# Kernel tuning notes

Measured on AMD Instinct MI355X. Metric: run time of the kernel, lower is better.

## Reference

```python
import jax, jax.numpy as jnp
import numpy as np

MAX_INT = 1e4  # sentinel used by the original (transitions into START / out of STOP forbidden)
VOCAB, E, H, T, B, S = 50257, 512, 1024, 50, 8, 512  # T = tagset_size + 2


def _lstm_scan(x, h0, c0, Wih, Whh, b):
    # x: [time, batch, E] (time axis is the ORIGINAL batch dim, faithful to the
    # torch code which feeds [B,S,E] into a batch_first=False LSTM)
    def step(carry, xt):
        h, c = carry
        g = xt @ Wih.T + h @ Whh.T + b
        i, f, gg, o = jnp.split(g, 4, axis=-1)  # torch gate order i,f,g,o
        c = jax.nn.sigmoid(f) * c + jax.nn.sigmoid(i) * jnp.tanh(gg)
        h = jax.nn.sigmoid(o) * jnp.tanh(c)
        return (h, c), h
    _, hs = jax.lax.scan(step, (h0, c0), x)
    return hs


def setup_inputs() -> dict:
    key = jax.random.key(0)
    k = jax.random.split(key, 14)
    Hd = H // 2
    X = jax.random.randint(k[0], (B, S), 0, VOCAB)
    Y = jax.random.randint(k[1], (B, S), 0, T - 2)  # real tags only (no start/stop)
    h0 = jax.random.normal(k[2], (2, S, Hd), jnp.float32)
    c0 = jax.random.normal(k[3], (2, S, Hd), jnp.float32)
    emb_table = jax.random.normal(k[4], (VOCAB, E), jnp.float32) * 0.02
    Wih_f = jax.random.normal(k[5], (4 * Hd, E), jnp.float32) * 0.05
    Whh_f = jax.random.normal(k[6], (4 * Hd, Hd), jnp.float32) * 0.05
    b_f = jnp.zeros((4 * Hd,), jnp.float32)
    Wih_b = jax.random.normal(k[7], (4 * Hd, E), jnp.float32) * 0.05
    Whh_b = jax.random.normal(k[8], (4 * Hd, Hd), jnp.float32) * 0.05
    b_b = jnp.zeros((4 * Hd,), jnp.float32)
    fc_W = jax.random.normal(k[9], (T, H), jnp.float32) * 0.05
    fc_b = jnp.zeros((T,), jnp.float32)
    tr = jax.random.normal(k[10], (T, T), jnp.float32)
    transitions = tr.at[-2, :].set(-MAX_INT).at[:, -1].set(-MAX_INT)
    return {"X": X, "Y": Y, "h0": h0, "c0": c0, "emb_table": emb_table,
            "Wih_f": Wih_f, "Whh_f": Whh_f, "b_f": b_f,
            "Wih_b": Wih_b, "Whh_b": Whh_b, "b_b": b_b,
            "fc_W": fc_W, "fc_b": fc_b, "transitions": transitions}


def reference(X, Y, h0, c0, emb_table, Wih_f, Whh_f, b_f, Wih_b, Whh_b, b_b, fc_W, fc_b, transitions):
    emb = emb_table[X]                                   # [B,S,E]
    # BiLSTM: torch sees axis0 as time (faithful quirk), hidden batch == S
    hf = _lstm_scan(emb, h0[0], c0[0], Wih_f, Whh_f, b_f)
    hb = _lstm_scan(emb[::-1], h0[1], c0[1], Wih_b, Whh_b, b_b)[::-1]
    lstm_out = jnp.concatenate([hf, hb], axis=-1)        # [B,S,H]
    feats = lstm_out @ fc_W.T + fc_b                     # [B,S,T]
    nB, Tt = X.shape[0], transitions.shape[0]
    # CRF forward algorithm (log partition), vectorized over tags
    init = jnp.full((nB, Tt), -MAX_INT, feats.dtype).at[:, -2].set(0.0)
    def crf_step(fv, feat):                              # fv [B,T], feat [B,T]
        nv = fv[:, None, :] + transitions[None, :, :] + feat[:, :, None]  # [B,next,prev]
        return jax.nn.logsumexp(nv, axis=2), None
    fv, _ = jax.lax.scan(crf_step, init, jnp.swapaxes(feats, 0, 1))
    forward_score = jax.nn.logsumexp(fv + transitions[-1][None, :], axis=1).sum()
    # gold path score
    start = jnp.full((nB, 1), Tt - 2, dtype=Y.dtype)
    tags = jnp.concatenate([start, Y], axis=1)           # [B,S+1]
    trans_sc = transitions[tags[:, 1:], tags[:, :-1]].sum()
    emit_sc = jnp.take_along_axis(feats, tags[:, 1:, None], axis=2)[..., 0].sum()
    gold_score = trans_sc + emit_sc + transitions[-1, tags[:, -1]].sum()
    score = forward_score - gold_score
    return score, Y
```

## Files before the change

### kernel.cpp

```cpp
#include <hip/hip_runtime.h>
#include <hip/hip_bf16.h>

typedef __attribute__((ext_vector_type(4))) float f32x4;
typedef __attribute__((ext_vector_type(8))) short short8;

#define LN2F 0.69314718055994531f

__device__ __forceinline__ unsigned short f2b(float x){
  union{float f;unsigned u;}v; v.f=x;
  unsigned r = v.u + 0x7fffu + ((v.u>>16)&1u);
  return (unsigned short)(r>>16);
}
__device__ __forceinline__ float b2f(unsigned short h){
  union{unsigned u;float f;}v; v.u = ((unsigned)h)<<16; return v.f;
}
__device__ __forceinline__ float sigm(float x){ return 1.f/(1.f+__expf(-x)); }
__device__ __forceinline__ float tanh_(float x){ float t=__expf(2.f*x); return 1.f - 2.f/(t+1.f); }

__device__ __forceinline__ void gll16(const void* g, void* l){
  __builtin_amdgcn_global_load_lds((const __attribute__((address_space(1))) void*)g,
                                   (__attribute__((address_space(3))) void*)l, 16, 0, 0);
}

__global__ __launch_bounds__(256) void prep_kernel(
  const int* __restrict__ X, const int* __restrict__ Y,
  const float* __restrict__ h0, const float* __restrict__ c0,
  const float* __restrict__ emb,
  const float* __restrict__ WihF, const float* __restrict__ WihB,
  const float* __restrict__ WhhFf, const float* __restrict__ WhhBf,
  const float* __restrict__ fcWf, const float* __restrict__ trans,
  unsigned short* __restrict__ Abf, unsigned short* __restrict__ Wcat,
  unsigned short* __restrict__ WhhF, unsigned short* __restrict__ WhhB,
  unsigned short* __restrict__ hbufs, float* __restrict__ cbuf,
  unsigned short* __restrict__ fcW, unsigned short* __restrict__ Ebf,
  float* __restrict__ out)
{
  const int tid = blockIdx.x*256 + threadIdx.x;
  const int nth = gridDim.x*256;
  if(tid==0) out[0] = 0.f;
  for(int i=tid;i<524288;i+=nth){
    int r = i>>7, q = i&127;
    float4 v = ((const float4*)(emb + (size_t)X[r]*512))[q];
    ushort4 o; o.x=f2b(v.x); o.y=f2b(v.y); o.z=f2b(v.z); o.w=f2b(v.w);
    ((ushort4*)Abf)[i] = o;
  }
  for(int i=tid;i<524288;i+=nth){
    int r = i>>7, q = i&127;
    const float* src = (r<2048) ? (WihF + (size_t)r*512) : (WihB + (size_t)(r-2048)*512);
    float4 v = ((const float4*)src)[q];
    ushort4 o; o.x=f2b(v.x); o.y=f2b(v.y); o.z=f2b(v.z); o.w=f2b(v.w);
    ((ushort4*)Wcat)[i] = o;
  }
  for(int i=tid;i<262144;i+=nth){
    float4 v = ((const float4*)WhhFf)[i];
    ushort4 o; o.x=f2b(v.x); o.y=f2b(v.y); o.z=f2b(v.z); o.w=f2b(v.w);
    ((ushort4*)WhhF)[i] = o;
  }
  for(int i=tid;i<262144;i+=nth){
    float4 v = ((const float4*)WhhBf)[i];
    ushort4 o; o.x=f2b(v.x); o.y=f2b(v.y); o.z=f2b(v.z); o.w=f2b(v.w);
    ((ushort4*)WhhB)[i] = o;
  }
  for(int i=tid;i<131072;i+=nth){
    int d = i>>16, rest = i&65535;
    float4 v = ((const float4*)h0)[i];
    ushort4 o; o.x=f2b(v.x); o.y=f2b(v.y); o.z=f2b(v.z); o.w=f2b(v.w);
    ((ushort4*)hbufs)[(size_t)(d*2)*65536 + rest] = o;
  }
  for(int i=tid;i<131072;i+=nth) ((float4*)cbuf)[i] = ((const float4*)c0)[i];
  for(int i=tid;i<16384;i+=nth){
    int n = i>>8, q = i&255;
    float4 v;
    if (n<50) v = ((const float4*)(fcWf + (size_t)n*1024))[q];
    else { v.x=0.f; v.y=0.f; v.z=0.f; v.w=0.f; }
    ushort4 o; o.x=f2b(v.x); o.y=f2b(v.y); o.z=f2b(v.z); o.w=f2b(v.w);
    ((ushort4*)fcW)[i] = o;
  }
  for(int i=tid;i<4096;i+=nth){
    int n = i>>6, p = i&63;
    float v = (n<50 && p<50) ? __expf(trans[n*50+p]) : 0.f;
    Ebf[i] = f2b(v);
  }
  for(int i=tid;i<4096;i+=nth) out[1+i] = (float)Y[i];
}

__global__ __launch_bounds__(256) void gemm1_kernel(const unsigned short* __restrict__ A,
                                                    const unsigned short* __restrict__ B,
                                                    unsigned short* __restrict__ C){
  __shared__ __align__(16) unsigned short SS[4][4][2][2048];
  const int t = threadIdx.x, w = t>>6, l = t&63;
  const int m0 = blockIdx.x<<7, n0 = blockIdx.y<<7;
  const int wr = (w>>1)<<6, wc = (w&1)<<6;
  const int fr = l&15, fk = (l>>4)<<3;
  const int sr = l>>2, c0 = (l&3)<<3;
  f32x4 acc[4][4];
  #pragma unroll
  for(int i=0;i<4;i++)
    #pragma unroll
    for(int j=0;j<4;j++) acc[i][j]=(f32x4)0.f;
  const unsigned short* Aw = A + (size_t)(m0+wr)*512;
  const unsigned short* Bw = B + (size_t)(n0+wc)*512;
#define G1STAGE(KT) { \
    unsigned short* pa_ = &SS[w][(KT)&3][0][0]; \
    unsigned short* pb_ = &SS[w][(KT)&3][1][0]; \
    const int kc_ = ((KT)<<5) + c0; \
    gll16(Aw + (size_t)(    sr)*512 + kc_, pa_); \
    gll16(Aw + (size_t)(16+sr)*512 + kc_, pa_+512); \
    gll16(Aw + (size_t)(32+sr)*512 + kc_, pa_+1024); \
    gll16(Aw + (size_t)(48+sr)*512 + kc_, pa_+1536); \
    gll16(Bw + (size_t)(    sr)*512 + kc_, pb_); \
    gll16(Bw + (size_t)(16+sr)*512 + kc_, pb_+512); \
    gll16(Bw + (size_t)(32+sr)*512 + kc_, pb_+1024); \
    gll16(Bw + (size_t)(48+sr)*512 + kc_, pb_+1536); \
  }
  G1STAGE(0) G1STAGE(1) G1STAGE(2)
#define G1STEP(KT, VM) { \
    if((KT)+3 < 16) G1STAGE((KT)+3) \
    asm volatile("s_waitcnt vmcnt(" VM ")" ::: "memory"); \
    const unsigned short* pa_ = &SS[w][(KT)&3][0][0]; \
    const unsigned short* pb_ = &SS[w][(KT)&3][1][0]; \
    short8 af_[4], bf_[4]; \
    _Pragma("unroll") \
    for(int mi=0;mi<4;mi++) af_[mi] = *(const short8*)(pa_ + mi*512 + fr*32 + fk); \
    _Pragma("unroll") \
    for(int ni=0;ni<4;ni++) bf_[ni] = *(const short8*)(pb_ + ni*512 + fr*32 + fk); \
    _Pragma("unroll") \
    for(int mi=0;mi<4;mi++) \
      _Pragma("unroll") \
      for(int ni=0;ni<4;ni++) \
        acc[mi][ni] = __builtin_amdgcn_mfma_f32_16x16x32_bf16(af_[mi], bf_[ni], acc[mi][ni], 0,0,0); \
  }
  G1STEP(0,"24")  G1STEP(1,"24")  G1STEP(2,"24")  G1STEP(3,"24")
  G1STEP(4,"24")  G1STEP(5,"24")  G1STEP(6,"24")  G1STEP(7,"24")
  G1STEP(8,"24")  G1STEP(9,"24")  G1STEP(10,"24") G1STEP(11,"24")
  G1STEP(12,"24") G1STEP(13,"16") G1STEP(14,"8")  G1STEP(15,"0")
#undef G1STEP
#undef G1STAGE
  #pragma unroll
  for(int mi=0;mi<4;mi++)
    #pragma unroll
    for(int ni=0;ni<4;ni++)
      #pragma unroll
      for(int j=0;j<4;j++){
        int row = m0 + wr + mi*16 + ((l>>4)<<2) + j;
        int col = n0 + wc + ni*16 + fr;
        C[(size_t)row*4096 + col] = f2b(acc[mi][ni][j]);
      }
}

__global__ __launch_bounds__(256) void lstm_step_kernel(
  unsigned short* __restrict__ hbufs, float* __restrict__ cbuf,
  unsigned short* __restrict__ hall, const unsigned short* __restrict__ Gin,
  const unsigned short* __restrict__ WhhF_, const unsigned short* __restrict__ WhhB_,
  const float* __restrict__ bF, const float* __restrict__ bB, int t)
{
  __shared__ __align__(16) unsigned short WL[16*4*64*8];
  __shared__ __align__(16) unsigned short Ab4[4][128*32];
  const int d = blockIdx.z;
  const int m0 = blockIdx.x<<7;
  const int u0 = blockIdx.y<<4;
  const int tin = d ? (7-t) : t;
  const int par = t&1;
  const unsigned short* hprev = hbufs + (size_t)(d*2+par)*262144;
  unsigned short* hnext = hbufs + (size_t)(d*2+(par^1))*262144;
  const unsigned short* W = d ? WhhB_ : WhhF_;
  const float* bias = d ? bB : bF;
  const int tx = threadIdx.x, w = tx>>6, l = tx&63;
  const int fr = l&15, q = l>>4, fk = q<<3;
  {
    const int row = tx >> 2, qq = tx & 3;
    const int g = row >> 4, ul = row & 15;
    const int grow = (g<<9) + u0 + ul;
    #pragma unroll
    for(int kt=0;kt<16;kt++){
      uint4 v = *(const uint4*)(W + (size_t)grow*512 + kt*32 + qq*8);
      *(uint4*)(WL + ((kt*4+g)*64 + (qq*16+ul))*8) = v;
    }
  }
  __syncthreads();
  f32x4 acc[2][4];
  #pragma unroll
  for(int i=0;i<2;i++)
    #pragma unroll
    for(int j=0;j<4;j++) acc[i][j]=(f32x4)0.f;
  const int r0 = (w<<5) + (l>>2), c0 = (l&3)<<3;
  const unsigned short* hA0 = hprev + (size_t)(m0+r0)*512;
  const unsigned short* hA1 = hprev + (size_t)(m0+r0+16)*512;
#define ABUF(i) (Ab4[(i)] + ((w<<5)*32))
  gll16(hA0 + 0*32 + c0, ABUF(0)); gll16(hA1 + 0*32 + c0, ABUF(0)+16*32);
  gll16(hA0 + 1*32 + c0, ABUF(1)); gll16(hA1 + 1*32 + c0, ABUF(1)+16*32);
  gll16(hA0 + 2*32 + c0, ABUF(2)); gll16(hA1 + 2*32 + c0, ABUF(2)+16*32);
#define LSTEP(KT, VM) {                                                       \
    if((KT)+3 < 16){                                                          \
      const int kc_ = ((KT)+3)*32 + c0;                                       \
      gll16(hA0 + kc_, ABUF(((KT)+3)&3));                                     \
      gll16(hA1 + kc_, ABUF(((KT)+3)&3)+16*32);                               \
    }                                                                         \
    asm volatile("s_waitcnt vmcnt(" VM ")" ::: "memory");                     \
    const unsigned short* cur_ = ABUF((KT)&3);                                \
    short8 a0_ = *(const short8*)(cur_ + fr*32 + fk);                         \
    short8 a1_ = *(const short8*)(cur_ + (16+fr)*32 + fk);                    \
    short8 bv_[4];                                                            \
    _Pragma("unroll")                                                         \
    for(int g=0;g<4;g++) bv_[g] = *(const short8*)(WL + (((KT)*4+g)*64 + l)*8);\
    _Pragma("unroll")                                                         \
    for(int g=0;g<4;g++){                                                     \
      acc[0][g] = __builtin_amdgcn_mfma_f32_16x16x32_bf16(a0_, bv_[g], acc[0][g], 0,0,0); \
      acc[1][g] = __builtin_amdgcn_mfma_f32_16x16x32_bf16(a1_, bv_[g], acc[1][g], 0,0,0); \
    }                                                                         \
  }
  LSTEP(0,"6")  LSTEP(1,"6")  LSTEP(2,"6")  LSTEP(3,"6")
  LSTEP(4,"6")  LSTEP(5,"6")  LSTEP(6,"6")  LSTEP(7,"6")
  LSTEP(8,"6")  LSTEP(9,"6")  LSTEP(10,"6") LSTEP(11,"6")
  LSTEP(12,"6") LSTEP(13,"4") LSTEP(14,"2") LSTEP(15,"0")
#undef LSTEP
#undef ABUF
  #pragma unroll
  for(int mi=0;mi<2;mi++)
    #pragma unroll
    for(int j=0;j<4;j++){
      int rs = m0 + w*32 + mi*16 + (q<<2) + j;
      int u  = u0 + fr;
      size_t grow = (size_t)(tin*512 + rs)*4096 + (size_t)d*2048;
      float p0 = acc[mi][0][j] + b2f(Gin[grow +    0 + u]) + bias[   0+u];
      float p1 = acc[mi][1][j] + b2f(Gin[grow +  512 + u]) + bias[ 512+u];
      float p2 = acc[mi][2][j] + b2f(Gin[grow + 1024 + u]) + bias[1024+u];
      float p3 = acc[mi][3][j] + b2f(Gin[grow + 1536 + u]) + bias[1536+u];
      size_t ci = (size_t)d*262144 + (size_t)rs*512 + u;
      float c = sigm(p1)*cbuf[ci] + sigm(p0)*tanh_(p2);
      cbuf[ci] = c;
      float h = sigm(p3)*tanh_(c);
      hnext[(size_t)rs*512+u] = f2b(h);
      hall[(size_t)(tin*512+rs)*1024 + (size_t)d*512 + u] = f2b(h);
    }
}

__global__ __launch_bounds__(256) void fc_kernel(const unsigned short* __restrict__ hA,
    const unsigned short* __restrict__ Wf, const float* __restrict__ fcb,
    float* __restrict__ feats){
  __shared__ __align__(16) unsigned short As[128*40];
  __shared__ __align__(16) unsigned short Bs[64*40];
  const int tx = threadIdx.x, w = tx>>6, l = tx&63;
  const int m0 = blockIdx.x<<7;
  const int srow = tx>>2, scol = (tx&3)<<3;
  const int fr=l&15, fk=(l>>4)<<3;
  f32x4 acc[2][4];
  #pragma unroll
  for(int i=0;i<2;i++)
    #pragma unroll
    for(int j=0;j<4;j++) acc[i][j]=(f32x4)0.f;
  uint4 pa0 = *(const uint4*)(hA + (size_t)(m0+srow)*1024 + scol);
  uint4 pa1 = *(const uint4*)(hA + (size_t)(m0+64+srow)*1024 + scol);
  uint4 pb0 = *(const uint4*)(Wf + (size_t)srow*1024 + scol);
  for(int kt=0; kt<32; ++kt){
    __syncthreads();
    *(uint4*)&As[srow*40+scol] = pa0;
    *(uint4*)&As[(64+srow)*40+scol] = pa1;
    *(uint4*)&Bs[srow*40+scol] = pb0;
    __syncthreads();
    if(kt<31){
      int kc = (kt+1)*32 + scol;
      pa0 = *(const uint4*)(hA + (size_t)(m0+srow)*1024 + kc);
      pa1 = *(const uint4*)(hA + (size_t)(m0+64+srow)*1024 + kc);
      pb0 = *(const uint4*)(Wf + (size_t)srow*1024 + kc);
    }
    short8 af[2], bf[4];
    #pragma unroll
    for(int mi=0;mi<2;mi++) af[mi] = *(const short8*)&As[(w*32+mi*16+fr)*40 + fk];
    #pragma unroll
    for(int ni=0;ni<4;ni++) bf[ni] = *(const short8*)&Bs[(ni*16+fr)*40 + fk];
    #pragma unroll
    for(int mi=0;mi<2;mi++)
      #pragma unroll
      for(int ni=0;ni<4;ni++)
        acc[mi][ni] = __builtin_amdgcn_mfma_f32_16x16x32_bf16(af[mi], bf[ni], acc[mi][ni], 0,0,0);
  }
  #pragma unroll
  for(int mi=0;mi<2;mi++)
    #pragma unroll
    for(int ni=0;ni<4;ni++)
      #pragma unroll
      for(int j=0;j<4;j++){
        int rs = m0 + w*32 + mi*16 + ((l>>4)<<2) + j;
        int n  = ni*16 + fr;
        feats[(size_t)rs*64+n] = acc[mi][ni][j] + (n<50 ? fcb[n] : 0.f);
      }
}

__global__ __launch_bounds__(64) void crf_group_kernel(
    const float* __restrict__ feats, const unsigned short* __restrict__ Ebf,
    float* __restrict__ Wout, int* __restrict__ kexp)
{
  __shared__ __align__(16) unsigned short PT[64*72];
  __shared__ float fe[32*64];
  const int g = blockIdx.x, b = blockIdx.y;
  const int l = threadIdx.x;
  const int lj = l & 15, q = l >> 4;
  const float* fb = feats + (size_t)(b*512 + g*32)*64;
  #pragma unroll
  for(int j=0;j<32;j++) fe[j*64 + l] = fb[j*64 + l];
  short8 afE[4][2];
  #pragma unroll
  for(int i=0;i<4;i++)
    #pragma unroll
    for(int h=0;h<2;h++)
      afE[i][h] = *(const short8*)(Ebf + (i*16+lj)*64 + h*32 + q*8);
  {
    uint4 erow[8];
    #pragma unroll
    for(int i=0;i<8;i++) erow[i] = *(const uint4*)(Ebf + l*64 + i*8);
    float ef0 = __expf(fe[l]);
    const unsigned* e32 = (const unsigned*)erow;
    #pragma unroll
    for(int m=0;m<64;m++){
      unsigned short eb = (unsigned short)(e32[m>>1] >> ((m&1)*16));
      PT[m*72 + l] = f2b(b2f(eb) * ef0);
    }
  }
  float sc_lag = 1.f;
  int exprev = 0, kblk = 0;
  for(int k=1;k<32;k++){
    kblk += exprev;
    float ev[4][4];
    #pragma unroll
    for(int i=0;i<4;i++)
      #pragma unroll
      for(int r=0;r<4;r++)
        ev[i][r] = __expf(fe[k*64 + i*16 + q*4 + r]) * sc_lag;
    short8 bfP[4][2];
    #pragma unroll
    for(int j=0;j<4;j++)
      #pragma unroll
      for(int h=0;h<2;h++)
        bfP[j][h] = *(const short8*)&PT[(j*16+lj)*72 + h*32 + q*8];
    f32x4 acc[4][4];
    #pragma unroll
    for(int i=0;i<4;i++)
      #pragma unroll
      for(int j=0;j<4;j++) acc[i][j] = (f32x4)0.f;
    #pragma unroll
    for(int h=0;h<2;h++)
      #pragma unroll
      for(int i=0;i<4;i++)
        #pragma unroll
        for(int j=0;j<4;j++)
          acc[i][j] = __builtin_amdgcn_mfma_f32_16x16x32_bf16(afE[i][h], bfP[j][h], acc[i][j], 0,0,0);
    float mx = 1e-30f;
    float* Wo = Wout + (size_t)(b*16 + g)*4096;
    #pragma unroll
    for(int i=0;i<4;i++)
      #pragma unroll
      for(int j=0;j<4;j++){
        float v0 = acc[i][j][0]*ev[i][0];
        float v1 = acc[i][j][1]*ev[i][1];
        float v2 = acc[i][j][2]*ev[i][2];
        float v3 = acc[i][j][3]*ev[i][3];
        mx = fmaxf(fmaxf(mx, fmaxf(v0,v1)), fmaxf(v2,v3));
        int base = (j*16+lj)*72 + i*16 + q*4;
        *(unsigned*)&PT[base]   = (unsigned)f2b(v0) | ((unsigned)f2b(v1)<<16);
        *(unsigned*)&PT[base+2] = (unsigned)f2b(v2) | ((unsigned)f2b(v3)<<16);
        if(k==31){
          int n = i*16 + q*4, m = j*16 + lj;
          Wo[(size_t)(n+0)*64 + m] = v0;
          Wo[(size_t)(n+1)*64 + m] = v1;
          Wo[(size_t)(n+2)*64 + m] = v2;
          Wo[(size_t)(n+3)*64 + m] = v3;
        }
      }
    #pragma unroll
    for(int off=1; off<64; off<<=1) mx = fmaxf(mx, __shfl_xor(mx, off));
    int ex = ((__builtin_bit_cast(int, mx) >> 23) & 0xff) - 127;
    ex = ex < -120 ? -120 : (ex > 120 ? 120 : ex);
    sc_lag = __builtin_bit_cast(float, (unsigned)((127-ex)<<23));
    exprev = ex;
  }
  if(l==0) kexp[b*16 + g] = kblk;
}

__global__ __launch_bounds__(256) void crf_seq_kernel(const float* __restrict__ W,
    const int* __restrict__ kexp, const float* __restrict__ trans,
    const float* __restrict__ feats, const int* __restrict__ Y,
    float* __restrict__ out){
  const int b = blockIdx.x;
  if(b < 8){
    if(threadIdx.x >= 64) return;
    __shared__ __align__(16) float sh[64];
    const int l = threadIdx.x;
    const float* Wb = W + (size_t)b*65536;
    float kl = (l<16) ? (float)kexp[b*16 + l] : 0.f;
    #pragma unroll
    for(int off=32;off;off>>=1) kl += __shfl_down(kl, off);
    float G = (l==48) ? 1.f : 0.f;
    float sc = 1.f, Mrun = 0.f;
    int exprev = 0;
    float4 curA[16], curB[16];
    #pragma unroll
    for(int i=0;i<16;i++) curA[i] = ((const float4*)(Wb + (size_t)l*64))[i];

#define SEQ_STEP(CUR, NXT, GI) {                                            \
    sh[l] = G;                                                              \
    const float* wn = Wb + (size_t)(((GI)+1)&15)*4096 + (size_t)l*64;       \
    _Pragma("unroll")                                                       \
    for(int i=0;i<16;i++) NXT[i] = ((const float4*)wn)[i];                  \
    float4 gq[16];                                                          \
    _Pragma("unroll")                                                       \
    for(int i=0;i<16;i++) gq[i] = ((const float4*)sh)[i];                   \
    float a0=0.f,a1=0.f,a2=0.f,a3=0.f;                                      \
    _Pragma("unroll")                                                       \
    for(int i=0;i<16;i++){                                                  \
      a0 = fmaf(CUR[i].x, gq[i].x, a0);                                     \
      a1 = fmaf(CUR[i].y, gq[i].y, a1);                                     \
      a2 = fmaf(CUR[i].z, gq[i].z, a2);                                     \
      a3 = fmaf(CUR[i].w, gq[i].w, a3);                                     \
    }                                                                       \
    float S = (a0+a1)+(a2+a3);                                              \
    Mrun += (float)exprev;                                                  \
    G = S * sc;                                                             \
    float Sp = __builtin_bit_cast(float, __builtin_amdgcn_readfirstlane(    \
                 __builtin_bit_cast(int, fmaxf(S, 1e-35f))));               \
    int ex = ((__builtin_bit_cast(int, Sp) >> 23) & 0xff) - 127;            \
    ex = ex < -120 ? -120 : (ex > 120 ? 120 : ex);                          \
    sc = __builtin_bit_cast(float, (unsigned)((127-ex)<<23));               \
    exprev = ex;                                                            \
  }

    for(int g=0; g<16; g+=2){
      SEQ_STEP(curA, curB, g)
      SEQ_STEP(curB, curA, g+1)
    }
#undef SEQ_STEP
    float u = (l<50) ? __expf(trans[49*50+l]) : 0.f;
    float val = G * u;
    #pragma unroll
    for(int off=32;off;off>>=1) val += __shfl_down(val, off);
    if(l==0) atomicAdd(out, logf(fmaxf(val,1e-35f)) + (Mrun + kl)*LN2F);
  } else {
    const int tx = threadIdx.x;
    float acc = 0.f;
    for(int i=tx; i<4096; i+=256){
      int s = i & 511;
      int y = Y[i];
      int prev = s ? Y[i-1] : 48;
      acc += trans[y*50+prev] + feats[(size_t)i*64+y];
      if (s==511) acc += trans[49*50+y];
    }
    #pragma unroll
    for(int off=32; off; off>>=1) acc += __shfl_down(acc, off);
    __shared__ float red[4];
    if((tx&63)==0) red[tx>>6] = acc;
    __syncthreads();
    if(tx==0) atomicAdd(out, -(red[0]+red[1]+red[2]+red[3]));
  }
}

extern "C" void kernel_launch(void* const* d_in, const int* in_sizes, int n_in,
                              void* d_out, int out_size, void* d_ws, size_t ws_size,
                              hipStream_t stream) {
  (void)in_sizes; (void)n_in; (void)out_size; (void)ws_size;
  const int*   X     = (const int*)d_in[0];
  const int*   Y     = (const int*)d_in[1];
  const float* h0    = (const float*)d_in[2];
  const float* c0    = (const float*)d_in[3];
  const float* emb   = (const float*)d_in[4];
  const float* WihF  = (const float*)d_in[5];
  const float* WhhFf = (const float*)d_in[6];
  const float* bF    = (const float*)d_in[7];
  const float* WihB  = (const float*)d_in[8];
  const float* WhhBf = (const float*)d_in[9];
  const float* bB    = (const float*)d_in[10];
  const float* fcWf  = (const float*)d_in[11];
  const float* fcb   = (const float*)d_in[12];
  const float* trans = (const float*)d_in[13];
  float* out = (float*)d_out;
  char* ws = (char*)d_ws;

  unsigned short* Abf   = (unsigned short*)(ws + 0);
  unsigned short* Wcat  = (unsigned short*)(ws + 4194304);
  unsigned short* WhhF  = (unsigned short*)(ws + 8388608);
  unsigned short* WhhB  = (unsigned short*)(ws + 10485760);
  unsigned short* Gin   = (unsigned short*)(ws + 12582912);
  float*          Wgrp  = (float*)(ws + 12582912);
  int*            kexp  = (int*)(ws + 20971520);
  unsigned short* hbufs = (unsigned short*)(ws + 46137344);
  float*          cbuf  = (float*)(ws + 48234496);
  unsigned short* hall  = (unsigned short*)(ws + 50331648);
  unsigned short* fcW   = (unsigned short*)(ws + 58720256);
  float*          feats = (float*)(ws + 58851328);
  unsigned short* Ebf   = (unsigned short*)(ws + 59900160);

  hipLaunchKernelGGL(prep_kernel, dim3(1024), dim3(256), 0, stream,
      X, Y, h0, c0, emb, WihF, WihB, WhhFf, WhhBf, fcWf, trans,
      Abf, Wcat, WhhF, WhhB, hbufs, cbuf, fcW, Ebf, out);
  hipLaunchKernelGGL(gemm1_kernel, dim3(32,32), dim3(256), 0, stream, Abf, Wcat, Gin);
  for(int t=0;t<8;t++)
    hipLaunchKernelGGL(lstm_step_kernel, dim3(4,32,2), dim3(256), 0, stream,
        hbufs, cbuf, hall, Gin, WhhF, WhhB, bF, bB, t);
  hipLaunchKernelGGL(fc_kernel, dim3(32), dim3(256), 0, stream, hall, fcW, fcb, feats);
  hipLaunchKernelGGL(crf_group_kernel, dim3(16,8), dim3(64), 0, stream, feats, Ebf, Wgrp, kexp);
  hipLaunchKernelGGL(crf_seq_kernel, dim3(9), dim3(256), 0, stream, Wgrp, kexp, trans, feats, Y, out);
}
```

Measured before the change: 192.5 us.

## Fuse input projection into LSTM steps and FC into CRF group kernel

Removes the standalone input-projection GEMM and its Gin buffer: each LSTM step kernel now also computes x_t·Wih over a 32-step K loop, holding both Wih and Whh slices in LDS with a 3-deep staging buffer. The FC projection is folded into crf_group_kernel, which now runs 256 threads to compute its feature tile with MFMA before one wave runs the CRF part. This saves two launches and the round-trip of the large bf16 gate tensor through global memory. In exchange, each of the 8 serial LSTM steps does twice the matmul work and uses more LDS, which may lengthen the critical path.

```diff
diff --git a/kernel.cpp b/kernel.cpp
--- a/kernel.cpp
+++ b/kernel.cpp
@@ -84,78 +84,16 @@
   for(int i=tid;i<4096;i+=nth) out[1+i] = (float)Y[i];
 }
 
-__global__ __launch_bounds__(256) void gemm1_kernel(const unsigned short* __restrict__ A,
-                                                    const unsigned short* __restrict__ B,
-                                                    unsigned short* __restrict__ C){
-  __shared__ __align__(16) unsigned short SS[4][4][2][2048];
-  const int t = threadIdx.x, w = t>>6, l = t&63;
-  const int m0 = blockIdx.x<<7, n0 = blockIdx.y<<7;
-  const int wr = (w>>1)<<6, wc = (w&1)<<6;
-  const int fr = l&15, fk = (l>>4)<<3;
-  const int sr = l>>2, c0 = (l&3)<<3;
-  f32x4 acc[4][4];
-  #pragma unroll
-  for(int i=0;i<4;i++)
-    #pragma unroll
-    for(int j=0;j<4;j++) acc[i][j]=(f32x4)0.f;
-  const unsigned short* Aw = A + (size_t)(m0+wr)*512;
-  const unsigned short* Bw = B + (size_t)(n0+wc)*512;
-#define G1STAGE(KT) { \
-    unsigned short* pa_ = &SS[w][(KT)&3][0][0]; \
-    unsigned short* pb_ = &SS[w][(KT)&3][1][0]; \
-    const int kc_ = ((KT)<<5) + c0; \
-    gll16(Aw + (size_t)(    sr)*512 + kc_, pa_); \
-    gll16(Aw + (size_t)(16+sr)*512 + kc_, pa_+512); \
-    gll16(Aw + (size_t)(32+sr)*512 + kc_, pa_+1024); \
-    gll16(Aw + (size_t)(48+sr)*512 + kc_, pa_+1536); \
-    gll16(Bw + (size_t)(    sr)*512 + kc_, pb_); \
-    gll16(Bw + (size_t)(16+sr)*512 + kc_, pb_+512); \
-    gll16(Bw + (size_t)(32+sr)*512 + kc_, pb_+1024); \
-    gll16(Bw + (size_t)(48+sr)*512 + kc_, pb_+1536); \
-  }
-  G1STAGE(0) G1STAGE(1) G1STAGE(2)
-#define G1STEP(KT, VM) { \
-    if((KT)+3 < 16) G1STAGE((KT)+3) \
-    asm volatile("s_waitcnt vmcnt(" VM ")" ::: "memory"); \
-    const unsigned short* pa_ = &SS[w][(KT)&3][0][0]; \
-    const unsigned short* pb_ = &SS[w][(KT)&3][1][0]; \
-    short8 af_[4], bf_[4]; \
-    _Pragma("unroll") \
-    for(int mi=0;mi<4;mi++) af_[mi] = *(const short8*)(pa_ + mi*512 + fr*32 + fk); \
-    _Pragma("unroll") \
-    for(int ni=0;ni<4;ni++) bf_[ni] = *(const short8*)(pb_ + ni*512 + fr*32 + fk); \
-    _Pragma("unroll") \
-    for(int mi=0;mi<4;mi++) \
-      _Pragma("unroll") \
-      for(int ni=0;ni<4;ni++) \
-        acc[mi][ni] = __builtin_amdgcn_mfma_f32_16x16x32_bf16(af_[mi], bf_[ni], acc[mi][ni], 0,0,0); \
-  }
-  G1STEP(0,"24")  G1STEP(1,"24")  G1STEP(2,"24")  G1STEP(3,"24")
-  G1STEP(4,"24")  G1STEP(5,"24")  G1STEP(6,"24")  G1STEP(7,"24")
-  G1STEP(8,"24")  G1STEP(9,"24")  G1STEP(10,"24") G1STEP(11,"24")
-  G1STEP(12,"24") G1STEP(13,"16") G1STEP(14,"8")  G1STEP(15,"0")
-#undef G1STEP
-#undef G1STAGE
-  #pragma unroll
-  for(int mi=0;mi<4;mi++)
-    #pragma unroll
-    for(int ni=0;ni<4;ni++)
-      #pragma unroll
-      for(int j=0;j<4;j++){
-        int row = m0 + wr + mi*16 + ((l>>4)<<2) + j;
-        int col = n0 + wc + ni*16 + fr;
-        C[(size_t)row*4096 + col] = f2b(acc[mi][ni][j]);
-      }
-}
-
 __global__ __launch_bounds__(256) void lstm_step_kernel(
   unsigned short* __restrict__ hbufs, float* __restrict__ cbuf,
-  unsigned short* __restrict__ hall, const unsigned short* __restrict__ Gin,
+  unsigned short* __restrict__ hall, const unsigned short* __restrict__ Abf,
+  const unsigned short* __restrict__ Wcat,
   const unsigned short* __restrict__ WhhF_, const unsigned short* __restrict__ WhhB_,
   const float* __restrict__ bF, const float* __restrict__ bB, int t)
 {
-  __shared__ __align__(16) unsigned short WL[16*4*64*8];
-  __shared__ __align__(16) unsigned short Ab4[4][128*32];
+  __shared__ __align__(16) unsigned short WLih[16*4*64*8];
+  __shared__ __align__(16) unsigned short WLhh[16*4*64*8];
+  __shared__ __align__(16) unsigned short Ab3[3][128*32];
   const int d = blockIdx.z;
   const int m0 = blockIdx.x<<7;
   const int u0 = blockIdx.y<<4;
@@ -163,7 +101,8 @@
   const int par = t&1;
   const unsigned short* hprev = hbufs + (size_t)(d*2+par)*262144;
   unsigned short* hnext = hbufs + (size_t)(d*2+(par^1))*262144;
-  const unsigned short* W = d ? WhhB_ : WhhF_;
+  const unsigned short* Wih = Wcat + (size_t)(d*2048)*512;
+  const unsigned short* Whh = d ? WhhB_ : WhhF_;
   const float* bias = d ? bB : bF;
   const int tx = threadIdx.x, w = tx>>6, l = tx&63;
   const int fr = l&15, q = l>>4, fk = q<<3;
@@ -173,8 +112,10 @@
     const int grow = (g<<9) + u0 + ul;
     #pragma unroll
     for(int kt=0;kt<16;kt++){
-      uint4 v = *(const uint4*)(W + (size_t)grow*512 + kt*32 + qq*8);
-      *(uint4*)(WL + ((kt*4+g)*64 + (qq*16+ul))*8) = v;
+      uint4 vi = *(const uint4*)(Wih + (size_t)grow*512 + kt*32 + qq*8);
+      *(uint4*)(WLih + ((kt*4+g)*64 + (qq*16+ul))*8) = vi;
+      uint4 vh = *(const uint4*)(Whh + (size_t)grow*512 + kt*32 + qq*8);
+      *(uint4*)(WLhh + ((kt*4+g)*64 + (qq*16+ul))*8) = vh;
     }
   }
   __syncthreads();
@@ -184,36 +125,44 @@
     #pragma unroll
     for(int j=0;j<4;j++) acc[i][j]=(f32x4)0.f;
   const int r0 = (w<<5) + (l>>2), c0 = (l&3)<<3;
+  const unsigned short* xA0 = Abf + (size_t)(tin*512 + m0 + r0)*512;
+  const unsigned short* xA1 = xA0 + (size_t)16*512;
   const unsigned short* hA0 = hprev + (size_t)(m0+r0)*512;
-  const unsigned short* hA1 = hprev + (size_t)(m0+r0+16)*512;
-#define ABUF(i) (Ab4[(i)] + ((w<<5)*32))
-  gll16(hA0 + 0*32 + c0, ABUF(0)); gll16(hA1 + 0*32 + c0, ABUF(0)+16*32);
-  gll16(hA0 + 1*32 + c0, ABUF(1)); gll16(hA1 + 1*32 + c0, ABUF(1)+16*32);
-  gll16(hA0 + 2*32 + c0, ABUF(2)); gll16(hA1 + 2*32 + c0, ABUF(2)+16*32);
-#define LSTEP(KT, VM) {                                                       \
-    if((KT)+3 < 16){                                                          \
-      const int kc_ = ((KT)+3)*32 + c0;                                       \
-      gll16(hA0 + kc_, ABUF(((KT)+3)&3));                                     \
-      gll16(hA1 + kc_, ABUF(((KT)+3)&3)+16*32);                               \
-    }                                                                         \
+  const unsigned short* hA1 = hA0 + (size_t)16*512;
+#define ABUF(i) (Ab3[(i)] + ((w<<5)*32))
+#define STAGE(T) { \
+    unsigned short* d_ = ABUF((T)%3); \
+    if((T)<16){ const int kc_=(T)*32+c0;      gll16(xA0+kc_, d_); gll16(xA1+kc_, d_+512); } \
+    else      { const int kc_=((T)-16)*32+c0; gll16(hA0+kc_, d_); gll16(hA1+kc_, d_+512); } \
+  }
+  STAGE(0) STAGE(1)
+#define LSTEP(T, VM) {                                                        \
+    if((T)+2 < 32) STAGE((T)+2)                                               \
     asm volatile("s_waitcnt vmcnt(" VM ")" ::: "memory");                     \
-    const unsigned short* cur_ = ABUF((KT)&3);                                \
+    const unsigned short* cur_ = ABUF((T)%3);                                 \
     short8 a0_ = *(const short8*)(cur_ + fr*32 + fk);                         \
     short8 a1_ = *(const short8*)(cur_ + (16+fr)*32 + fk);                    \
+    const unsigned short* WL_ = ((T)<16) ? WLih : WLhh;                       \
+    const int kk_ = (T)&15;                                                   \
     short8 bv_[4];                                                            \
     _Pragma("unroll")                                                         \
-    for(int g=0;g<4;g++) bv_[g] = *(const short8*)(WL + (((KT)*4+g)*64 + l)*8);\
+    for(int g=0;g<4;g++) bv_[g] = *(const short8*)(WL_ + ((kk_*4+g)*64 + l)*8);\
     _Pragma("unroll")                                                         \
     for(int g=0;g<4;g++){                                                     \
       acc[0][g] = __builtin_amdgcn_mfma_f32_16x16x32_bf16(a0_, bv_[g], acc[0][g], 0,0,0); \
       acc[1][g] = __builtin_amdgcn_mfma_f32_16x16x32_bf16(a1_, bv_[g], acc[1][g], 0,0,0); \
     }                                                                         \
   }
-  LSTEP(0,"6")  LSTEP(1,"6")  LSTEP(2,"6")  LSTEP(3,"6")
-  LSTEP(4,"6")  LSTEP(5,"6")  LSTEP(6,"6")  LSTEP(7,"6")
-  LSTEP(8,"6")  LSTEP(9,"6")  LSTEP(10,"6") LSTEP(11,"6")
-  LSTEP(12,"6") LSTEP(13,"4") LSTEP(14,"2") LSTEP(15,"0")
+  LSTEP(0,"4")  LSTEP(1,"4")  LSTEP(2,"4")  LSTEP(3,"4")
+  LSTEP(4,"4")  LSTEP(5,"4")  LSTEP(6,"4")  LSTEP(7,"4")
+  LSTEP(8,"4")  LSTEP(9,"4")  LSTEP(10,"4") LSTEP(11,"4")
+  LSTEP(12,"4") LSTEP(13,"4") LSTEP(14,"4") LSTEP(15,"4")
+  LSTEP(16,"4") LSTEP(17,"4") LSTEP(18,"4") LSTEP(19,"4")
+  LSTEP(20,"4") LSTEP(21,"4") LSTEP(22,"4") LSTEP(23,"4")
+  LSTEP(24,"4") LSTEP(25,"4") LSTEP(26,"4") LSTEP(27,"4")
+  LSTEP(28,"4") LSTEP(29,"4") LSTEP(30,"2") LSTEP(31,"0")
 #undef LSTEP
+#undef STAGE
 #undef ABUF
   #pragma unroll
   for(int mi=0;mi<2;mi++)
@@ -221,11 +170,10 @@
     for(int j=0;j<4;j++){
       int rs = m0 + w*32 + mi*16 + (q<<2) + j;
       int u  = u0 + fr;
-      size_t grow = (size_t)(tin*512 + rs)*4096 + (size_t)d*2048;
-      float p0 = acc[mi][0][j] + b2f(Gin[grow +    0 + u]) + bias[   0+u];
-      float p1 = acc[mi][1][j] + b2f(Gin[grow +  512 + u]) + bias[ 512+u];
-      float p2 = acc[mi][2][j] + b2f(Gin[grow + 1024 + u]) + bias[1024+u];
-      float p3 = acc[mi][3][j] + b2f(Gin[grow + 1536 + u]) + bias[1536+u];
+      float p0 = acc[mi][0][j] + bias[   0+u];
+      float p1 = acc[mi][1][j] + bias[ 512+u];
+      float p2 = acc[mi][2][j] + bias[1024+u];
+      float p3 = acc[mi][3][j] + bias[1536+u];
       size_t ci = (size_t)d*262144 + (size_t)rs*512 + u;
       float c = sigm(p1)*cbuf[ci] + sigm(p0)*tanh_(p2);
       cbuf[ci] = c;
@@ -235,70 +183,44 @@
     }
 }
 
-__global__ __launch_bounds__(256) void fc_kernel(const unsigned short* __restrict__ hA,
-    const unsigned short* __restrict__ Wf, const float* __restrict__ fcb,
-    float* __restrict__ feats){
-  __shared__ __align__(16) unsigned short As[128*40];
-  __shared__ __align__(16) unsigned short Bs[64*40];
-  const int tx = threadIdx.x, w = tx>>6, l = tx&63;
-  const int m0 = blockIdx.x<<7;
-  const int srow = tx>>2, scol = (tx&3)<<3;
-  const int fr=l&15, fk=(l>>4)<<3;
-  f32x4 acc[2][4];
-  #pragma unroll
-  for(int i=0;i<2;i++)
-    #pragma unroll
-    for(int j=0;j<4;j++) acc[i][j]=(f32x4)0.f;
-  uint4 pa0 = *(const uint4*)(hA + (size_t)(m0+srow)*1024 + scol);
-  uint4 pa1 = *(const uint4*)(hA + (size_t)(m0+64+srow)*1024 + scol);
-  uint4 pb0 = *(const uint4*)(Wf + (size_t)srow*1024 + scol);
-  for(int kt=0; kt<32; ++kt){
-    __syncthreads();
-    *(uint4*)&As[srow*40+scol] = pa0;
-    *(uint4*)&As[(64+srow)*40+scol] = pa1;
-    *(uint4*)&Bs[srow*40+scol] = pb0;
-    __syncthreads();
-    if(kt<31){
-      int kc = (kt+1)*32 + scol;
-      pa0 = *(const uint4*)(hA + (size_t)(m0+srow)*1024 + kc);
-      pa1 = *(const uint4*)(hA + (size_t)(m0+64+srow)*1024 + kc);
-      pb0 = *(const uint4*)(Wf + (size_t)srow*1024 + kc);
-    }
-    short8 af[2], bf[4];
-    #pragma unroll
-    for(int mi=0;mi<2;mi++) af[mi] = *(const short8*)&As[(w*32+mi*16+fr)*40 + fk];
-    #pragma unroll
-    for(int ni=0;ni<4;ni++) bf[ni] = *(const short8*)&Bs[(ni*16+fr)*40 + fk];
-    #pragma unroll
-    for(int mi=0;mi<2;mi++)
-      #pragma unroll
-      for(int ni=0;ni<4;ni++)
-        acc[mi][ni] = __builtin_amdgcn_mfma_f32_16x16x32_bf16(af[mi], bf[ni], acc[mi][ni], 0,0,0);
-  }
-  #pragma unroll
-  for(int mi=0;mi<2;mi++)
-    #pragma unroll
-    for(int ni=0;ni<4;ni++)
-      #pragma unroll
-      for(int j=0;j<4;j++){
-        int rs = m0 + w*32 + mi*16 + ((l>>4)<<2) + j;
-        int n  = ni*16 + fr;
-        feats[(size_t)rs*64+n] = acc[mi][ni][j] + (n<50 ? fcb[n] : 0.f);
-      }
-}
-
-__global__ __launch_bounds__(64) void crf_group_kernel(
-    const float* __restrict__ feats, const unsigned short* __restrict__ Ebf,
-    float* __restrict__ Wout, int* __restrict__ kexp)
+__global__ __launch_bounds__(256) void crf_group_kernel(
+    const unsigned short* __restrict__ hall, const unsigned short* __restrict__ fcWp,
+    const float* __restrict__ fcb, const unsigned short* __restrict__ Ebf,
+    float* __restrict__ feats, float* __restrict__ Wout, int* __restrict__ kexp)
 {
   __shared__ __align__(16) unsigned short PT[64*72];
   __shared__ float fe[32*64];
   const int g = blockIdx.x, b = blockIdx.y;
-  const int l = threadIdx.x;
+  const int tx = threadIdx.x, w = tx>>6, l = tx&63;
   const int lj = l & 15, q = l >> 4;
-  const float* fb = feats + (size_t)(b*512 + g*32)*64;
-  #pragma unroll
-  for(int j=0;j<32;j++) fe[j*64 + l] = fb[j*64 + l];
+  {
+    const int R0 = b*512 + g*32;
+    const int wr = (w>>1)<<4, wc = (w&1)<<5;
+    f32x4 acf0 = (f32x4)0.f, acf1 = (f32x4)0.f;
+    const unsigned short* Ar  = hall + (size_t)(R0+wr+lj)*1024;
+    const unsigned short* Br0 = fcWp + (size_t)(wc+lj)*1024;
+    const unsigned short* Br1 = fcWp + (size_t)(wc+16+lj)*1024;
+    #pragma unroll 8
+    for(int kt=0; kt<32; kt++){
+      short8 a  = *(const short8*)(Ar  + kt*32 + q*8);
+      short8 b0 = *(const short8*)(Br0 + kt*32 + q*8);
+      short8 b1 = *(const short8*)(Br1 + kt*32 + q*8);
+      acf0 = __builtin_amdgcn_mfma_f32_16x16x32_bf16(a, b0, acf0, 0,0,0);
+      acf1 = __builtin_amdgcn_mfma_f32_16x16x32_bf16(a, b1, acf1, 0,0,0);
+    }
+    #pragma unroll
+    for(int j=0;j<4;j++){
+      int row = wr + q*4 + j;
+      int n0 = wc + lj, n1 = wc + 16 + lj;
+      float v0 = acf0[j] + (n0<50 ? fcb[n0] : 0.f);
+      float v1 = acf1[j] + (n1<50 ? fcb[n1] : 0.f);
+      fe[row*64 + n0] = v0; fe[row*64 + n1] = v1;
+      feats[(size_t)(R0+row)*64 + n0] = v0;
+      feats[(size_t)(R0+row)*64 + n1] = v1;
+    }
+  }
+  __syncthreads();
+  if(w) return;
   short8 afE[4][2];
   #pragma unroll
   for(int i=0;i<4;i++)
@@ -478,7 +400,6 @@
   unsigned short* Wcat  = (unsigned short*)(ws + 4194304);
   unsigned short* WhhF  = (unsigned short*)(ws + 8388608);
   unsigned short* WhhB  = (unsigned short*)(ws + 10485760);
-  unsigned short* Gin   = (unsigned short*)(ws + 12582912);
   float*          Wgrp  = (float*)(ws + 12582912);
   int*            kexp  = (int*)(ws + 20971520);
   unsigned short* hbufs = (unsigned short*)(ws + 46137344);
@@ -491,11 +412,10 @@
   hipLaunchKernelGGL(prep_kernel, dim3(1024), dim3(256), 0, stream,
       X, Y, h0, c0, emb, WihF, WihB, WhhFf, WhhBf, fcWf, trans,
       Abf, Wcat, WhhF, WhhB, hbufs, cbuf, fcW, Ebf, out);
-  hipLaunchKernelGGL(gemm1_kernel, dim3(32,32), dim3(256), 0, stream, Abf, Wcat, Gin);
   for(int t=0;t<8;t++)
     hipLaunchKernelGGL(lstm_step_kernel, dim3(4,32,2), dim3(256), 0, stream,
-        hbufs, cbuf, hall, Gin, WhhF, WhhB, bF, bB, t);
-  hipLaunchKernelGGL(fc_kernel, dim3(32), dim3(256), 0, stream, hall, fcW, fcb, feats);
-  hipLaunchKernelGGL(crf_group_kernel, dim3(16,8), dim3(64), 0, stream, feats, Ebf, Wgrp, kexp);
+        hbufs, cbuf, hall, Abf, Wcat, WhhF, WhhB, bF, bB, t);
+  hipLaunchKernelGGL(crf_group_kernel, dim3(16,8), dim3(256), 0, stream,
+      hall, fcW, fcb, Ebf, feats, Wgrp, kexp);
   hipLaunchKernelGGL(crf_seq_kernel, dim3(9), dim3(256), 0, stream, Wgrp, kexp, trans, feats, Y, out);
 }
```

After: 197.8 us. 2.7% more time.
